# Kernel optimization log

Measured on AMD Instinct MI355X. Metric: run time of the kernel, lower is better.

The kernel has to match this reference:

```python
import jax, jax.numpy as jnp
import numpy as np

B, S, D, K = 32, 512, 512, 2048
NHEADS, NHASH, HLEN = 8, 4, 16
COMMIT = 0.25


def _conv1d(x, w, b):
    # x: [B, C, S], w: [O, I, k] (torch Conv1d layout), 'same' padding for odd k
    k = w.shape[-1]
    y = jax.lax.conv_general_dilated(x, w, (1,), [(k // 2, k // 2)],
                                     dimension_numbers=('NCH', 'OIH', 'NCH'))
    return y + b[None, :, None]


def _mha(x, in_w, in_b, out_w, out_b, nheads):
    # torch nn.MultiheadAttention (batch_first) with packed in_proj
    b, s, d = x.shape
    dh = d // nheads
    qkv = x @ in_w.T + in_b
    q, k, v = jnp.split(qkv, 3, axis=-1)
    sp = lambda t: t.reshape(b, s, nheads, dh).transpose(0, 2, 1, 3)
    q, k, v = sp(q), sp(k), sp(v)
    attn = jax.nn.softmax(jnp.einsum('bhqd,bhkd->bhqk', q, k) * (dh ** -0.5), axis=-1)
    o = jnp.einsum('bhqk,bhkd->bhqd', attn, v).transpose(0, 2, 1, 3).reshape(b, s, d)
    return o @ out_w.T + out_b


def setup_inputs() -> dict:
    key = jax.random.key(0)
    ks = jax.random.split(key, 16)
    w = lambda k, shape, s=0.02: jax.random.normal(k, shape, jnp.float32) * s
    z = lambda *shape: jnp.zeros(shape, jnp.float32)
    return {
        'market_data': jax.random.normal(ks[0], (B, S, D), jnp.float32),
        'W_in': w(ks[1], (D, D)), 'b_in': z(D),
        'pos_enc': w(ks[2], (S, D)),
        'conv3_w': w(ks[3], (D, D, 3)), 'conv3_b': z(D),
        'conv5_w': w(ks[4], (D, D, 5)), 'conv5_b': z(D),
        'conv7_w': w(ks[5], (D, D, 7)), 'conv7_b': z(D),
        'conv9_w': w(ks[6], (D, D, 9)), 'conv9_b': z(D),
        'ms_proj_w': w(ks[7], (D, 4 * D)), 'ms_proj_b': z(D),
        'in_proj_w': w(ks[8], (3 * D, D)), 'in_proj_b': z(3 * D),
        'attn_out_w': w(ks[9], (D, D)), 'attn_out_b': z(D),
        'codebook': jax.random.uniform(ks[10], (K, D), jnp.float32, -1.0 / K, 1.0 / K),
        'hash_w': w(ks[11], (NHASH, HLEN, D), 1.0),
        'reg1_w': w(ks[12], (D // 2, D)), 'reg1_b': z(D // 2),
        'reg2_w': w(ks[13], (K, D // 2)), 'reg2_b': z(K),
    }


def reference(market_data, W_in, b_in, pos_enc, conv3_w, conv3_b, conv5_w, conv5_b,
              conv7_w, conv7_b, conv9_w, conv9_b, ms_proj_w, ms_proj_b,
              in_proj_w, in_proj_b, attn_out_w, attn_out_b, codebook, hash_w,
              reg1_w, reg1_b, reg2_w, reg2_b):
    # input projection
    x = market_data @ W_in.T + b_in                                   # [B,S,D]
    # --- subsequence encoder ---
    xp = x + pos_enc[:x.shape[1]][None]
    xt = xp.transpose(0, 2, 1)                                        # [B,D,S]
    scales = [jax.nn.relu(_conv1d(xt, cw, cb)).transpose(0, 2, 1)
              for cw, cb in ((conv3_w, conv3_b), (conv5_w, conv5_b),
                             (conv7_w, conv7_b), (conv9_w, conv9_b))]
    multi = jnp.concatenate(scales, axis=-1)                          # [B,S,4D]
    proj = multi @ ms_proj_w.T + ms_proj_b                            # [B,S,D]
    enc = proj + _mha(proj, in_proj_w, in_proj_b, attn_out_w, attn_out_b, NHEADS)
    # --- vector quantizer (eval mode: no EMA update) ---
    flat = enc.reshape(-1, D)                                         # [N,D]
    dist = (jnp.sum(flat * flat, axis=1, keepdims=True)
            + jnp.sum(codebook * codebook, axis=1)
            - 2.0 * (flat @ codebook.T))                              # [N,K]
    idx = jnp.argmin(dist, axis=1)                                    # [N]
    quant = codebook[idx].reshape(enc.shape)
    commit = jnp.mean((jax.lax.stop_gradient(quant) - enc) ** 2)
    cb_loss = jnp.mean((quant - jax.lax.stop_gradient(enc)) ** 2)
    vq_loss = COMMIT * commit + cb_loss
    quant_st = enc + jax.lax.stop_gradient(quant - enc)               # straight-through
    # --- hash encoder on semantic ids ---
    hash_codes = (jnp.einsum('bsd,nhd->bsnh', quant_st, hash_w) > 0).astype(jnp.float32)
    # --- regime classifier ---
    h = jax.nn.relu(quant_st @ reg1_w.T + reg1_b)
    regime = jax.nn.softmax(h @ reg2_w.T + reg2_b, axis=-1)
    return (quant_st, vq_loss, idx.reshape(enc.shape[:-1]), hash_codes, regime)
```

## Files before the change

kernel.cpp:

```cpp
#include <hip/hip_runtime.h>
#include <hip/hip_bf16.h>


#define GF_BIAS 1
#define GF_RELU 2
#define GF_ADDP 4
#define GF_POS  8
#define GF_ACCP 16
#define GF_QSCALE 32

typedef _Float16 f16x8 __attribute__((ext_vector_type(8)));
typedef float    f32x4 __attribute__((ext_vector_type(4)));

static constexpr long long O_QUANT = 0LL;
static constexpr long long O_LOSS  = 8388608LL;
static constexpr long long O_IDX   = 8388609LL;
static constexpr long long O_HASH  = 8404993LL;
static constexpr long long O_REG   = 9453569LL;
static constexpr long long O_END   = 43008001LL;

static constexpr long long W_XP    = 0LL;
static constexpr long long W_CT    = 8388608LL;
static constexpr long long W_PROJ  = 16777216LL;
static constexpr long long W_VW    = 25165824LL;
static constexpr long long W_HREG  = 33554432LL;
static constexpr long long W_T     = 34078720LL;
static constexpr long long W_IDX   = 34209792LL;
static constexpr long long W_ASUM  = 34226176LL;
static constexpr long long W_CBB   = 34258944LL;
static constexpr long long W_LPART = 34263040LL;
static constexpr long long W_PBV   = 34271232LL;
static constexpr long long W_PBI   = 34336768LL;
static constexpr long long W_END   = 34402304LL;

__device__ __forceinline__ unsigned int pack_hl(float x)
{
    _Float16 h = (_Float16)x;
    float hf = (float)h;
    _Float16 l = (_Float16)(x - hf);
    unsigned short hb = __builtin_bit_cast(unsigned short, h);
    unsigned short lb = __builtin_bit_cast(unsigned short, l);
    return (unsigned int)hb | ((unsigned int)lb << 16);
}

__device__ __forceinline__ void split2(float x, unsigned short& h, unsigned short& l)
{
    _Float16 hf = (_Float16)x;
    _Float16 lf = (_Float16)(x - (float)hf);
    h = __builtin_bit_cast(unsigned short, hf);
    l = __builtin_bit_cast(unsigned short, lf);
}

__device__ __forceinline__ float unpack_sum(unsigned int u)
{
    _Float16 h = __builtin_bit_cast(_Float16, (unsigned short)(u & 0xffff));
    _Float16 l = __builtin_bit_cast(_Float16, (unsigned short)(u >> 16));
    return (float)h + (float)l;
}

__global__ __launch_bounds__(256)
void split_hl_r23(const float* __restrict__ src, unsigned int* __restrict__ dst)
{
    long long i = (long long)blockIdx.x*256 + threadIdx.x;
    dst[i] = pack_hl(src[i]);
}

__global__ __launch_bounds__(256)
void split_cb_r23(const float* __restrict__ cb, unsigned int* __restrict__ cbhl)
{
    long long i = (long long)blockIdx.x*256 + threadIdx.x;
    cbhl[i] = pack_hl(cb[i] * 2048.0f);
}

template<int KT>
__global__ __launch_bounds__(256)
void conv_w_tr_r23(const float* __restrict__ w, unsigned int* __restrict__ wt)
{
    long long i = (long long)blockIdx.x*256 + threadIdx.x;
    int o  = (int)(i / (512*KT));
    int rem= (int)(i % (512*KT));
    int t  = rem >> 9;
    int ii = rem & 511;
    wt[i] = pack_hl(w[(long long)o*512*KT + (long long)ii*KT + t]);
}

template<int KT>
__global__ __launch_bounds__(256)
void conv_mfma_r23(const unsigned int* __restrict__ xphl,
                   const unsigned int* __restrict__ wthl,
                   const float* __restrict__ bias, unsigned int* __restrict__ outp)
{
    constexpr int PAD = KT / 2;
    __shared__ unsigned short Ah[136][40];
    __shared__ unsigned short Al[136][40];
    __shared__ unsigned short Bh[128][40];
    __shared__ unsigned short Bl[128][40];
    const int tid  = threadIdx.x;
    const int lane = tid & 63;
    const int wave = tid >> 6;
    const int wm = (wave >> 1) * 64, wn = (wave & 1) * 64;
    const int bm = blockIdx.x * 128, bn = blockIdx.y * 128;
    const int l15 = lane & 15;
    const int lk8 = (lane >> 4) * 8;
    const int rbase = (lane >> 4) * 4;
    const int sb = bm & 511;
    const int brow0 = tid >> 3, bc = tid & 7;

    f32x4 acc[4][4];
    #pragma unroll
    for (int i=0;i<4;i++)
        #pragma unroll
        for (int j=0;j<4;j++)
            acc[i][j] = (f32x4){0.f,0.f,0.f,0.f};

    for (int i0 = 0; i0 < 512; i0 += 32) {
        __syncthreads();
        for (int sl = tid; sl < 136*8; sl += 256) {
            const int row = sl >> 3, c = sl & 7;
            const int srow = sb + row - 4;
            uint4 v = make_uint4(0u,0u,0u,0u);
            if (srow >= 0 && srow < 512)
                v = *(const uint4*)(xphl + (long long)(bm + row - 4)*512 + i0 + c*4);
            Ah[row][c*4+0] = (unsigned short)(v.x & 0xffff);
            Ah[row][c*4+1] = (unsigned short)(v.y & 0xffff);
            Ah[row][c*4+2] = (unsigned short)(v.z & 0xffff);
            Ah[row][c*4+3] = (unsigned short)(v.w & 0xffff);
            Al[row][c*4+0] = (unsigned short)(v.x >> 16);
            Al[row][c*4+1] = (unsigned short)(v.y >> 16);
            Al[row][c*4+2] = (unsigned short)(v.z >> 16);
            Al[row][c*4+3] = (unsigned short)(v.w >> 16);
        }
        uint4 vb[4];
        #pragma unroll
        for (int q = 0; q < 4; ++q) {
            const int row = brow0 + q*32;
            vb[q] = *(const uint4*)(wthl + (long long)(bn + row)*(KT*512) + 0*512 + i0 + bc*4);
        }
        for (int t = 0; t < KT; ++t) {
            #pragma unroll
            for (int q = 0; q < 4; ++q) {
                const int row = brow0 + q*32;
                Bh[row][bc*4+0] = (unsigned short)(vb[q].x & 0xffff);
                Bh[row][bc*4+1] = (unsigned short)(vb[q].y & 0xffff);
                Bh[row][bc*4+2] = (unsigned short)(vb[q].z & 0xffff);
                Bh[row][bc*4+3] = (unsigned short)(vb[q].w & 0xffff);
                Bl[row][bc*4+0] = (unsigned short)(vb[q].x >> 16);
                Bl[row][bc*4+1] = (unsigned short)(vb[q].y >> 16);
                Bl[row][bc*4+2] = (unsigned short)(vb[q].z >> 16);
                Bl[row][bc*4+3] = (unsigned short)(vb[q].w >> 16);
            }
            if (t + 1 < KT) {
                #pragma unroll
                for (int q = 0; q < 4; ++q) {
                    const int row = brow0 + q*32;
                    vb[q] = *(const uint4*)(wthl + (long long)(bn + row)*(KT*512) + (t+1)*512 + i0 + bc*4);
                }
            }
            __syncthreads();
            const int tofs = t - PAD + 4;
            f16x8 ah[4], al[4], bh[4], bl[4];
            #pragma unroll
            for (int mi = 0; mi < 4; ++mi) {
                ah[mi] = *(const f16x8*)(&Ah[wm + mi*16 + l15 + tofs][lk8]);
                al[mi] = *(const f16x8*)(&Al[wm + mi*16 + l15 + tofs][lk8]);
            }
            #pragma unroll
            for (int nj = 0; nj < 4; ++nj) {
                bh[nj] = *(const f16x8*)(&Bh[wn + nj*16 + l15][lk8]);
                bl[nj] = *(const f16x8*)(&Bl[wn + nj*16 + l15][lk8]);
            }
            #pragma unroll
            for (int mi = 0; mi < 4; ++mi)
                #pragma unroll
                for (int nj = 0; nj < 4; ++nj) {
                    acc[mi][nj] = __builtin_amdgcn_mfma_f32_16x16x32_f16(ah[mi], bh[nj], acc[mi][nj], 0, 0, 0);
                    acc[mi][nj] = __builtin_amdgcn_mfma_f32_16x16x32_f16(ah[mi], bl[nj], acc[mi][nj], 0, 0, 0);
                    acc[mi][nj] = __builtin_amdgcn_mfma_f32_16x16x32_f16(al[mi], bh[nj], acc[mi][nj], 0, 0, 0);
                }
            if (t + 1 < KT) __syncthreads();
        }
    }
    #pragma unroll
    for (int mi = 0; mi < 4; ++mi) {
        #pragma unroll
        for (int nj = 0; nj < 4; ++nj) {
            const int col = bn + wn + nj*16 + l15;
            const float bcol = bias[col];
            #pragma unroll
            for (int r = 0; r < 4; ++r) {
                const int row = bm + wm + mi*16 + rbase + r;
                float v = acc[mi][nj][r] + bcol;
                outp[(long long)row*512 + col] = pack_hl(fmaxf(v, 0.0f));
            }
        }
    }
}

template<int FLAGS>
__global__ __launch_bounds__(256)
void gemm_hl_r23(const unsigned int* __restrict__ A, const unsigned int* __restrict__ Bm,
                 const float* __restrict__ bias, const float* __restrict__ pos,
                 const unsigned int* __restrict__ addsrc, unsigned int* __restrict__ C,
                 int Kdim, int lda, int ldb, int ldc)
{
    __shared__ unsigned short Ah[128][40];
    __shared__ unsigned short Al[128][40];
    __shared__ unsigned short Bh[128][40];
    __shared__ unsigned short Bl[128][40];
    const int tid  = threadIdx.x;
    const int lane = tid & 63;
    const int wave = tid >> 6;
    const int wm = (wave >> 1) * 64, wn = (wave & 1) * 64;
    const int bm = blockIdx.x * 128, bn = blockIdx.y * 128;
    const int l15 = lane & 15;
    const int lk8 = (lane >> 4) * 8;
    const int rbase = (lane >> 4) * 4;
    const int cg   = tid & 7;
    const int rw0  = tid >> 3;

    f32x4 acc[4][4];
    #pragma unroll
    for (int i=0;i<4;i++)
        #pragma unroll
        for (int j=0;j<4;j++)
            acc[i][j] = (f32x4){0.f,0.f,0.f,0.f};

    uint4 va[4], vb[4];
    #pragma unroll
    for (int q = 0; q < 4; ++q) {
        const int row = rw0 + q*32;
        va[q] = *(const uint4*)(A  + (long long)(bm + row)*lda + cg*4);
        vb[q] = *(const uint4*)(Bm + (long long)(bn + row)*ldb + cg*4);
    }

    for (int k0 = 0; k0 < Kdim; k0 += 32) {
        __syncthreads();
        #pragma unroll
        for (int q = 0; q < 4; ++q) {
            const int row = rw0 + q*32;
            Ah[row][cg*4+0] = (unsigned short)(va[q].x & 0xffff);
            Ah[row][cg*4+1] = (unsigned short)(va[q].y & 0xffff);
            Ah[row][cg*4+2] = (unsigned short)(va[q].z & 0xffff);
            Ah[row][cg*4+3] = (unsigned short)(va[q].w & 0xffff);
            Al[row][cg*4+0] = (unsigned short)(va[q].x >> 16);
            Al[row][cg*4+1] = (unsigned short)(va[q].y >> 16);
            Al[row][cg*4+2] = (unsigned short)(va[q].z >> 16);
            Al[row][cg*4+3] = (unsigned short)(va[q].w >> 16);
            Bh[row][cg*4+0] = (unsigned short)(vb[q].x & 0xffff);
            Bh[row][cg*4+1] = (unsigned short)(vb[q].y & 0xffff);
            Bh[row][cg*4+2] = (unsigned short)(vb[q].z & 0xffff);
            Bh[row][cg*4+3] = (unsigned short)(vb[q].w & 0xffff);
            Bl[row][cg*4+0] = (unsigned short)(vb[q].x >> 16);
            Bl[row][cg*4+1] = (unsigned short)(vb[q].y >> 16);
            Bl[row][cg*4+2] = (unsigned short)(vb[q].z >> 16);
            Bl[row][cg*4+3] = (unsigned short)(vb[q].w >> 16);
        }
        if (k0 + 32 < Kdim) {
            #pragma unroll
            for (int q = 0; q < 4; ++q) {
                const int row = rw0 + q*32;
                va[q] = *(const uint4*)(A  + (long long)(bm + row)*lda + k0 + 32 + cg*4);
                vb[q] = *(const uint4*)(Bm + (long long)(bn + row)*ldb + k0 + 32 + cg*4);
            }
        }
        __syncthreads();
        f16x8 ah[4], al[4], bh[4], bl[4];
        #pragma unroll
        for (int mi = 0; mi < 4; ++mi) {
            ah[mi] = *(const f16x8*)(&Ah[wm + mi*16 + l15][lk8]);
            al[mi] = *(const f16x8*)(&Al[wm + mi*16 + l15][lk8]);
        }
        #pragma unroll
        for (int nj = 0; nj < 4; ++nj) {
            bh[nj] = *(const f16x8*)(&Bh[wn + nj*16 + l15][lk8]);
            bl[nj] = *(const f16x8*)(&Bl[wn + nj*16 + l15][lk8]);
        }
        #pragma unroll
        for (int mi = 0; mi < 4; ++mi)
            #pragma unroll
            for (int nj = 0; nj < 4; ++nj) {
                acc[mi][nj] = __builtin_amdgcn_mfma_f32_16x16x32_f16(ah[mi], bh[nj], acc[mi][nj], 0, 0, 0);
                acc[mi][nj] = __builtin_amdgcn_mfma_f32_16x16x32_f16(ah[mi], bl[nj], acc[mi][nj], 0, 0, 0);
                acc[mi][nj] = __builtin_amdgcn_mfma_f32_16x16x32_f16(al[mi], bh[nj], acc[mi][nj], 0, 0, 0);
            }
    }
    #pragma unroll
    for (int mi = 0; mi < 4; ++mi) {
        #pragma unroll
        for (int nj = 0; nj < 4; ++nj) {
            const int col = bn + wn + nj*16 + l15;
            #pragma unroll
            for (int r = 0; r < 4; ++r) {
                const int row = bm + wm + mi*16 + rbase + r;
                float v = acc[mi][nj][r];
                if constexpr (FLAGS & GF_BIAS) v += bias[col];
                if constexpr (FLAGS & GF_POS)  v += pos[(long long)(row & 511)*512 + col];
                if constexpr (FLAGS & GF_ADDP) v += unpack_sum(addsrc[(long long)row*ldc + col]);
                if constexpr (FLAGS & GF_ACCP) v += unpack_sum(C[(long long)row*ldc + col]);
                if constexpr (FLAGS & GF_QSCALE) v *= 0.125f;
                C[(long long)row*ldc + col] = pack_hl(v);
            }
        }
    }
}

__global__ __launch_bounds__(256)
void attn_mfma_r23(const unsigned int* __restrict__ Qbuf, const unsigned int* __restrict__ Kbuf,
                   const unsigned int* __restrict__ Vbuf, unsigned int* __restrict__ att)
{
    __shared__ unsigned short Qh[64][68];
    __shared__ unsigned short Ql[64][68];
    __shared__ unsigned short Kh[64][68];
    __shared__ unsigned short Kl[64][68];
    __shared__ unsigned short Vh[64][68];
    __shared__ unsigned short Vl[64][68];
    const int tid  = threadIdx.x;
    const int lane = tid & 63;
    const int wave = tid >> 6;
    const int l15  = lane & 15;
    const int lq   = lane >> 4;
    const int lq8  = lq * 8;
    const int bid = blockIdx.x;
    const int qt = bid & 7, h = (bid >> 3) & 7, b = bid >> 6;
    const int row0 = b*512 + qt*64;

    #pragma unroll
    for (int u = 0; u < 16; ++u) {
        int e = u*256 + tid;
        int r = e >> 6, c = e & 63;
        unsigned int uq = Qbuf[(long long)(row0 + r)*512 + h*64 + c];
        Qh[r][c] = (unsigned short)(uq & 0xffff);
        Ql[r][c] = (unsigned short)(uq >> 16);
    }

    float m[4], l[4];
    f32x4 accO[4];
    #pragma unroll
    for (int r=0;r<4;r++){ m[r] = -1e30f; l[r] = 0.f; }
    #pragma unroll
    for (int j=0;j<4;j++) accO[j] = (f32x4){0.f,0.f,0.f,0.f};

    for (int kv = 0; kv < 512; kv += 64) {
        __syncthreads();
        #pragma unroll
        for (int u = 0; u < 16; ++u) {
            int e = u*256 + tid;
            int r = e >> 6, c = e & 63;
            unsigned int uk = Kbuf[(long long)(b*512 + kv + r)*512 + h*64 + c];
            unsigned int uv = Vbuf[(long long)(b*512 + kv + r)*512 + h*64 + c];
            Kh[r][c] = (unsigned short)(uk & 0xffff);
            Kl[r][c] = (unsigned short)(uk >> 16);
            Vh[c][r] = (unsigned short)(uv & 0xffff);
            Vl[c][r] = (unsigned short)(uv >> 16);
        }
        __syncthreads();
        f32x4 accS[4];
        #pragma unroll
        for (int j=0;j<4;j++) accS[j] = (f32x4){0.f,0.f,0.f,0.f};
        #pragma unroll
        for (int ks = 0; ks < 2; ++ks) {
            f16x8 qh = *(const f16x8*)(&Qh[wave*16 + l15][ks*32 + lq8]);
            f16x8 ql = *(const f16x8*)(&Ql[wave*16 + l15][ks*32 + lq8]);
            #pragma unroll
            for (int nj = 0; nj < 4; ++nj) {
                f16x8 kh = *(const f16x8*)(&Kh[nj*16 + l15][ks*32 + lq8]);
                f16x8 kl = *(const f16x8*)(&Kl[nj*16 + l15][ks*32 + lq8]);
                accS[nj] = __builtin_amdgcn_mfma_f32_16x16x32_f16(qh, kh, accS[nj], 0, 0, 0);
                accS[nj] = __builtin_amdgcn_mfma_f32_16x16x32_f16(qh, kl, accS[nj], 0, 0, 0);
                accS[nj] = __builtin_amdgcn_mfma_f32_16x16x32_f16(ql, kh, accS[nj], 0, 0, 0);
            }
        }
        #pragma unroll
        for (int r = 0; r < 4; ++r) {
            float tm = fmaxf(fmaxf(accS[0][r], accS[1][r]), fmaxf(accS[2][r], accS[3][r]));
            #pragma unroll
            for (int msk = 1; msk < 16; msk <<= 1) tm = fmaxf(tm, __shfl_xor(tm, msk, 64));
            float mn = fmaxf(m[r], tm);
            float scale = expf(m[r] - mn);
            float rs = 0.f;
            #pragma unroll
            for (int nj = 0; nj < 4; ++nj) {
                float p = expf(accS[nj][r] - mn);
                accS[nj][r] = p;
                rs += p;
            }
            #pragma unroll
            for (int msk = 1; msk < 16; msk <<= 1) rs += __shfl_xor(rs, msk, 64);
            l[r] = l[r]*scale + rs;
            m[r] = mn;
            #pragma unroll
            for (int nj = 0; nj < 4; ++nj) accO[nj][r] *= scale;
        }
        __syncthreads();
        #pragma unroll
        for (int r = 0; r < 4; ++r)
            #pragma unroll
            for (int nj = 0; nj < 4; ++nj) {
                unsigned short hs, ls;
                split2(accS[nj][r], hs, ls);
                Kh[wave*16 + lq*4 + r][nj*16 + l15] = hs;
                Kl[wave*16 + lq*4 + r][nj*16 + l15] = ls;
            }
        __syncthreads();
        #pragma unroll
        for (int ks = 0; ks < 2; ++ks) {
            f16x8 ph = *(const f16x8*)(&Kh[wave*16 + l15][ks*32 + lq8]);
            f16x8 pl = *(const f16x8*)(&Kl[wave*16 + l15][ks*32 + lq8]);
            #pragma unroll
            for (int nj = 0; nj < 4; ++nj) {
                f16x8 vh = *(const f16x8*)(&Vh[nj*16 + l15][ks*32 + lq8]);
                f16x8 vl = *(const f16x8*)(&Vl[nj*16 + l15][ks*32 + lq8]);
                accO[nj] = __builtin_amdgcn_mfma_f32_16x16x32_f16(ph, vh, accO[nj], 0, 0, 0);
                accO[nj] = __builtin_amdgcn_mfma_f32_16x16x32_f16(ph, vl, accO[nj], 0, 0, 0);
                accO[nj] = __builtin_amdgcn_mfma_f32_16x16x32_f16(pl, vh, accO[nj], 0, 0, 0);
            }
        }
    }
    #pragma unroll
    for (int nj = 0; nj < 4; ++nj)
        #pragma unroll
        for (int r = 0; r < 4; ++r) {
            const int row = row0 + wave*16 + lq*4 + r;
            att[(long long)row*512 + h*64 + nj*16 + l15] = pack_hl(accO[nj][r] / l[r]);
        }
}

__global__ __launch_bounds__(256)
void row_sumsq_r23(const float* __restrict__ X, double* __restrict__ outp)
{
    const int row  = blockIdx.x*4 + (threadIdx.x >> 6);
    const int lane = threadIdx.x & 63;
    double s = 0.0;
    #pragma unroll
    for (int u = 0; u < 8; ++u) {
        float v = X[(long long)row*512 + lane + u*64];
        s += (double)v * (double)v;
    }
    #pragma unroll
    for (int msk = 32; msk; msk >>= 1) s += __shfl_xor(s, msk, 64);
    if (lane == 0) outp[row] = s;
}

__global__ __launch_bounds__(256)
void row_sumsq_hl_r23(const unsigned int* __restrict__ X, double* __restrict__ outp)
{
    const int row  = blockIdx.x*4 + (threadIdx.x >> 6);
    const int lane = threadIdx.x & 63;
    double s = 0.0;
    #pragma unroll
    for (int u = 0; u < 8; ++u) {
        float v = unpack_sum(X[(long long)row*512 + lane + u*64]);
        s += (double)v * (double)v;
    }
    #pragma unroll
    for (int msk = 32; msk; msk >>= 1) s += __shfl_xor(s, msk, 64);
    if (lane == 0) outp[row] = s;
}

__global__ __launch_bounds__(256)
void vq_argmin_mfma_r23(const unsigned int* __restrict__ enchl,
                        const unsigned int* __restrict__ cbhl,
                        const double* __restrict__ Asum, const double* __restrict__ cbB,
                        float* __restrict__ pbv, int* __restrict__ pbi)
{
    __shared__ unsigned int smem[10240];
    unsigned short* AhP = (unsigned short*)smem;
    unsigned short* AlP = AhP + 128*40;
    unsigned short* BhP = AlP + 128*40;
    unsigned short* BlP = BhP + 128*40;
    float* bvsP = (float*)smem;
    int*   bisP = (int*)(smem + 4096);

    const int tid  = threadIdx.x;
    const int lane = tid & 63;
    const int wave = tid >> 6;
    const int wm = (wave >> 1) * 64, wn = (wave & 1) * 64;
    const int bm = blockIdx.x * 128;
    const int l15 = lane & 15;
    const int lk8 = (lane >> 4) * 8;
    const int rbase = (lane >> 4) * 4;
    const int cg   = tid & 7;
    const int rw0  = tid >> 3;

    float bestv[16]; int besti[16];
    #pragma unroll
    for (int g = 0; g < 16; ++g) { bestv[g] = 3.0e38f; besti[g] = 2048; }

    for (int nb = 0; nb < 4; ++nb) {
        const int ct0 = blockIdx.y * 512 + nb * 128;
        f32x4 acc[4][4];
        #pragma unroll
        for (int i=0;i<4;i++)
            #pragma unroll
            for (int j=0;j<4;j++)
                acc[i][j] = (f32x4){0.f,0.f,0.f,0.f};

        uint4 va[4], vb[4];
        #pragma unroll
        for (int q = 0; q < 4; ++q) {
            const int row = rw0 + q*32;
            va[q] = *(const uint4*)(enchl + (long long)(bm + row)*512 + cg*4);
            vb[q] = *(const uint4*)(cbhl  + (long long)(ct0 + row)*512 + cg*4);
        }

        for (int k0 = 0; k0 < 512; k0 += 32) {
            __syncthreads();
            #pragma unroll
            for (int q = 0; q < 4; ++q) {
                const int row = rw0 + q*32;
                AhP[row*40 + cg*4+0] = (unsigned short)(va[q].x & 0xffff);
                AhP[row*40 + cg*4+1] = (unsigned short)(va[q].y & 0xffff);
                AhP[row*40 + cg*4+2] = (unsigned short)(va[q].z & 0xffff);
                AhP[row*40 + cg*4+3] = (unsigned short)(va[q].w & 0xffff);
                AlP[row*40 + cg*4+0] = (unsigned short)(va[q].x >> 16);
                AlP[row*40 + cg*4+1] = (unsigned short)(va[q].y >> 16);
                AlP[row*40 + cg*4+2] = (unsigned short)(va[q].z >> 16);
                AlP[row*40 + cg*4+3] = (unsigned short)(va[q].w >> 16);
                BhP[row*40 + cg*4+0] = (unsigned short)(vb[q].x & 0xffff);
                BhP[row*40 + cg*4+1] = (unsigned short)(vb[q].y & 0xffff);
                BhP[row*40 + cg*4+2] = (unsigned short)(vb[q].z & 0xffff);
                BhP[row*40 + cg*4+3] = (unsigned short)(vb[q].w & 0xffff);
                BlP[row*40 + cg*4+0] = (unsigned short)(vb[q].x >> 16);
                BlP[row*40 + cg*4+1] = (unsigned short)(vb[q].y >> 16);
                BlP[row*40 + cg*4+2] = (unsigned short)(vb[q].z >> 16);
                BlP[row*40 + cg*4+3] = (unsigned short)(vb[q].w >> 16);
            }
            if (k0 + 32 < 512) {
                #pragma unroll
                for (int q = 0; q < 4; ++q) {
                    const int row = rw0 + q*32;
                    va[q] = *(const uint4*)(enchl + (long long)(bm + row)*512 + k0 + 32 + cg*4);
                    vb[q] = *(const uint4*)(cbhl  + (long long)(ct0 + row)*512 + k0 + 32 + cg*4);
                }
            }
            __syncthreads();
            f16x8 ah[4], al[4], bh[4], bl[4];
            #pragma unroll
            for (int mi = 0; mi < 4; ++mi) {
                ah[mi] = *(const f16x8*)(&AhP[(wm + mi*16 + l15)*40 + lk8]);
                al[mi] = *(const f16x8*)(&AlP[(wm + mi*16 + l15)*40 + lk8]);
            }
            #pragma unroll
            for (int nj = 0; nj < 4; ++nj) {
                bh[nj] = *(const f16x8*)(&BhP[(wn + nj*16 + l15)*40 + lk8]);
                bl[nj] = *(const f16x8*)(&BlP[(wn + nj*16 + l15)*40 + lk8]);
            }
            #pragma unroll
            for (int mi = 0; mi < 4; ++mi)
                #pragma unroll
                for (int nj = 0; nj < 4; ++nj) {
                    acc[mi][nj] = __builtin_amdgcn_mfma_f32_16x16x32_f16(ah[mi], bh[nj], acc[mi][nj], 0, 0, 0);
                    acc[mi][nj] = __builtin_amdgcn_mfma_f32_16x16x32_f16(ah[mi], bl[nj], acc[mi][nj], 0, 0, 0);
                    acc[mi][nj] = __builtin_amdgcn_mfma_f32_16x16x32_f16(al[mi], bh[nj], acc[mi][nj], 0, 0, 0);
                }
        }
        #pragma unroll
        for (int mi = 0; mi < 4; ++mi) {
            #pragma unroll
            for (int r = 0; r < 4; ++r) {
                const int g = mi*4 + r;
                const float anf = (float)Asum[bm + wm + mi*16 + rbase + r];
                #pragma unroll
                for (int nj = 0; nj < 4; ++nj) {
                    const int col = ct0 + wn + nj*16 + l15;
                    const float bf = (float)cbB[col];
                    const float s1 = anf + bf;
                    const float dot = acc[mi][nj][r] * (1.0f/2048.0f);
                    const float df  = 2.0f * dot;
                    const float qd  = s1 - df;
                    if (qd < bestv[g] || (qd == bestv[g] && col < besti[g])) {
                        bestv[g] = qd; besti[g] = col;
                    }
                }
            }
        }
    }
    __syncthreads();
    #pragma unroll
    for (int mi = 0; mi < 4; ++mi)
        #pragma unroll
        for (int r = 0; r < 4; ++r) {
            const int row  = wm + mi*16 + rbase + r;
            const int slot = (wave & 1)*16 + l15;
            bvsP[row*32 + slot] = bestv[mi*4 + r];
            bisP[row*32 + slot] = besti[mi*4 + r];
        }
    __syncthreads();
    if (tid < 128) {
        float bv = bvsP[tid*32]; int bi = bisP[tid*32];
        #pragma unroll
        for (int s = 1; s < 32; ++s) {
            float v = bvsP[tid*32 + s]; int ii = bisP[tid*32 + s];
            if (v < bv || (v == bv && ii < bi)) { bv = v; bi = ii; }
        }
        pbv[(long long)blockIdx.y*16384 + bm + tid] = bv;
        pbi[(long long)blockIdx.y*16384 + bm + tid] = bi;
    }
}

__global__ __launch_bounds__(256)
void vq_reduce_r23(const float* __restrict__ pbv, const int* __restrict__ pbi,
                   int* __restrict__ idxout, float* __restrict__ out)
{
    int n = blockIdx.x*256 + threadIdx.x;
    if (n >= 16384) return;
    float bv = pbv[n]; int bi = pbi[n];
    #pragma unroll
    for (int q = 1; q < 4; ++q) {
        float v = pbv[q*16384 + n]; int ii = pbi[q*16384 + n];
        if (v < bv || (v == bv && ii < bi)) { bv = v; bi = ii; }
    }
    int ci = bi & 2047;
    idxout[n] = ci;
    out[O_IDX + n] = (float)ci;
}

__global__ __launch_bounds__(256)
void vq_loss_partial_r23(const unsigned int* __restrict__ enchl,
                         const float* __restrict__ cb,
                         const int* __restrict__ idxp, double* __restrict__ part)
{
    __shared__ double red[4];
    const int row  = blockIdx.x*4 + (threadIdx.x >> 6);
    const int lane = threadIdx.x & 63;
    const int ci = idxp[row] & 2047;
    double s = 0.0;
    #pragma unroll
    for (int u = 0; u < 8; ++u) {
        int d = lane + u*64;
        float e = unpack_sum(enchl[(long long)row*512 + d]);
        double dv = (double)cb[(long long)ci*512 + d] - (double)e;
        s += dv * dv;
    }
    #pragma unroll
    for (int msk = 32; msk; msk >>= 1) s += __shfl_xor(s, msk, 64);
    if (lane == 0) red[threadIdx.x >> 6] = s;
    __syncthreads();
    if (threadIdx.x == 0)
        part[blockIdx.x] = red[0] + red[1] + red[2] + red[3];
}

template<int FLAGS>
__global__ __launch_bounds__(256)
void gemm_bt_r23(const float* __restrict__ A, const float* __restrict__ Bm,
                 const float* __restrict__ bias, const float* __restrict__ pos,
                 const float* __restrict__ addsrc, float* __restrict__ C,
                 int Kdim, int lda, int ldb, int ldc)
{
    __shared__ float As[16][132];
    __shared__ float Bs[16][132];
    const int tid = threadIdx.x;
    const int tx = tid & 15, ty = tid >> 4;
    const int bm = blockIdx.x * 128, bn = blockIdx.y * 128;
    const int r0 = tid >> 2;
    const int kg = (tid & 3) << 2;
    const float* Arow0 = A  + (long long)(bm + r0) * lda + kg;
    const float* Arow1 = A  + (long long)(bm + r0 + 64) * lda + kg;
    const float* Brow0 = Bm + (long long)(bn + r0) * ldb + kg;
    const float* Brow1 = Bm + (long long)(bn + r0 + 64) * ldb + kg;

    float acc[8][8] = {};
    for (int k0 = 0; k0 < Kdim; k0 += 16) {
        float4 a0 = *(const float4*)(Arow0 + k0);
        float4 a1 = *(const float4*)(Arow1 + k0);
        float4 b0 = *(const float4*)(Brow0 + k0);
        float4 b1 = *(const float4*)(Brow1 + k0);
        __syncthreads();
        As[kg+0][r0]=a0.x; As[kg+1][r0]=a0.y; As[kg+2][r0]=a0.z; As[kg+3][r0]=a0.w;
        As[kg+0][r0+64]=a1.x; As[kg+1][r0+64]=a1.y; As[kg+2][r0+64]=a1.z; As[kg+3][r0+64]=a1.w;
        Bs[kg+0][r0]=b0.x; Bs[kg+1][r0]=b0.y; Bs[kg+2][r0]=b0.z; Bs[kg+3][r0]=b0.w;
        Bs[kg+0][r0+64]=b1.x; Bs[kg+1][r0+64]=b1.y; Bs[kg+2][r0+64]=b1.z; Bs[kg+3][r0+64]=b1.w;
        __syncthreads();
        #pragma unroll
        for (int kk = 0; kk < 16; ++kk) {
            float a[8], b[8];
            #pragma unroll
            for (int i=0;i<8;i++) a[i] = As[kk][ty*8+i];
            #pragma unroll
            for (int j=0;j<4;j++) b[j]   = Bs[kk][tx*4+j];
            #pragma unroll
            for (int j=0;j<4;j++) b[4+j] = Bs[kk][64+tx*4+j];
            #pragma unroll
            for (int i=0;i<8;i++)
                #pragma unroll
                for (int j=0;j<8;j++)
                    acc[i][j] = fmaf(a[i], b[j], acc[i][j]);
        }
    }
    #pragma unroll
    for (int i=0;i<8;i++){
        const int row = bm + ty*8 + i;
        #pragma unroll
        for (int j=0;j<8;j++){
            const int col = bn + ((j < 4) ? (tx*4 + j) : (64 + tx*4 + (j-4)));
            float v = acc[i][j];
            if constexpr (FLAGS & GF_BIAS) v += bias[col];
            if constexpr (FLAGS & GF_RELU) v = fmaxf(v, 0.0f);
            C[(long long)row*ldc + col] = v;
        }
    }
}

__global__ __launch_bounds__(256)
void softmax_rows_r23(float* __restrict__ R)
{
    const int row = blockIdx.x;
    const int tid = threadIdx.x;
    __shared__ float  redf[256];
    __shared__ double redd[256];
    float* p = R + (long long)row * 2048;
    float mx = -1e30f;
    for (int c = tid; c < 2048; c += 256) mx = fmaxf(mx, p[c]);
    redf[tid] = mx; __syncthreads();
    for (int s2 = 128; s2; s2 >>= 1) { if (tid < s2) redf[tid] = fmaxf(redf[tid], redf[tid+s2]); __syncthreads(); }
    mx = redf[0];
    double sum = 0.0;
    for (int c = tid; c < 2048; c += 256) { float e = expf(p[c] - mx); p[c] = e; sum += e; }
    redd[tid] = sum; __syncthreads();
    for (int s2 = 128; s2; s2 >>= 1) { if (tid < s2) redd[tid] += redd[tid+s2]; __syncthreads(); }
    double tot = redd[0];
    for (int c = tid; c < 2048; c += 256) p[c] = (float)((double)p[c] / tot);
}

__global__ __launch_bounds__(256)
void hash_table_r23(const float* __restrict__ cb, const float* __restrict__ hw,
                    float* __restrict__ T)
{
    const int k = blockIdx.x*4 + (threadIdx.x >> 6);
    const int j = threadIdx.x & 63;
    double s = 0.0;
    for (int d = 0; d < 512; ++d)
        s += (double)cb[(long long)k*512 + d] * (double)hw[(long long)j*512 + d];
    T[(long long)k*64 + j] = (s > 0.0) ? 1.0f : 0.0f;
}

__global__ void write_loss_r23(const double* __restrict__ part,
                               float* __restrict__ out)
{
    __shared__ double red[256];
    double s = 0.0;
    for (int i = threadIdx.x; i < 4096; i += 256) s += part[i];
    red[threadIdx.x] = s; __syncthreads();
    for (int s2 = 128; s2; s2 >>= 1) {
        if (threadIdx.x < s2) red[threadIdx.x] += red[threadIdx.x + s2];
        __syncthreads();
    }
    if (threadIdx.x == 0)
        out[O_LOSS] = (float)(1.25 * red[0] / 8388608.0);
}

__global__ __launch_bounds__(256)
void write_regime_r23(const float* __restrict__ R, const int* __restrict__ idxp,
                      float* __restrict__ out)
{
    long long i = (long long)blockIdx.x*256 + threadIdx.x;
    if (i >= 33554432LL) return;
    int n = (int)(i >> 11), c = (int)(i & 2047);
    int ci = idxp[n] & 2047;
    out[O_REG + i] = R[(long long)ci*2048 + c];
}

__global__ __launch_bounds__(256)
void write_hash_r23(const float* __restrict__ T, const int* __restrict__ idxp,
                    float* __restrict__ out)
{
    long long i = (long long)blockIdx.x*256 + threadIdx.x;
    if (i >= 1048576LL) return;
    int n = (int)(i >> 6), j = (int)(i & 63);
    int ci = idxp[n] & 2047;
    out[O_HASH + i] = T[(long long)ci*64 + j];
}

__global__ __launch_bounds__(256)
void write_quant_r23(const float* __restrict__ cb, const int* __restrict__ idxp,
                     float* __restrict__ out)
{
    long long i = (long long)blockIdx.x*256 + threadIdx.x;
    if (i >= 8388608LL) return;
    int n = (int)(i >> 9), d = (int)(i & 511);
    int ci = idxp[n] & 2047;
    out[O_QUANT + i] = cb[(long long)ci*512 + d];
}

extern "C" void kernel_launch(void* const* d_in, const int* in_sizes, int n_in,
                              void* d_out, int out_size, void* d_ws, size_t ws_size,
                              hipStream_t stream)
{
    (void)in_sizes; (void)n_in; (void)out_size;
    const float* market = (const float*)d_in[0];
    const float* W_in   = (const float*)d_in[1];
    const float* b_in   = (const float*)d_in[2];
    const float* pos    = (const float*)d_in[3];
    const float* c3w = (const float*)d_in[4];  const float* c3b = (const float*)d_in[5];
    const float* c5w = (const float*)d_in[6];  const float* c5b = (const float*)d_in[7];
    const float* c7w = (const float*)d_in[8];  const float* c7b = (const float*)d_in[9];
    const float* c9w = (const float*)d_in[10]; const float* c9b = (const float*)d_in[11];
    const float* msw = (const float*)d_in[12]; const float* msb = (const float*)d_in[13];
    const float* inw = (const float*)d_in[14]; const float* inb = (const float*)d_in[15];
    const float* aow = (const float*)d_in[16]; const float* aob = (const float*)d_in[17];
    const float* cb  = (const float*)d_in[18]; const float* hw  = (const float*)d_in[19];
    const float* r1w = (const float*)d_in[20]; const float* r1b = (const float*)d_in[21];
    const float* r2w = (const float*)d_in[22]; const float* r2b = (const float*)d_in[23];

    if (ws_size < (size_t)W_END * sizeof(float)) return;

    float* ws = (float*)d_ws;
    unsigned int* xphl   = (unsigned int*)(ws + W_XP);
    unsigned int* cthl   = (unsigned int*)(ws + W_CT);
    unsigned int* projhl = (unsigned int*)(ws + W_PROJ);
    unsigned int* vwbase = (unsigned int*)(ws + W_VW);
    unsigned int* wt3 = vwbase;
    unsigned int* wt5 = wt3 + 512*512*3;
    unsigned int* wt7 = wt5 + 512*512*5;
    unsigned int* wt9 = wt7 + 512*512*7;
    unsigned int* mswhl  = vwbase + 6291456;
    unsigned int* winhl  = mswhl + 1048576;
    unsigned int* inwqhl = winhl + 262144;
    unsigned int* inwkhl = inwqhl + 262144;
    unsigned int* vhl    = vwbase;
    unsigned int* inwvhl = (unsigned int*)(ws + W_HREG);
    unsigned int* aowhl  = inwvhl + 262144;
    float* hregp = ws + W_HREG;
    float* Tp    = ws + W_T;
    int*    idxp  = (int*)(ws + W_IDX);
    double* asump = (double*)(ws + W_ASUM);
    double* cbbp  = (double*)(ws + W_CBB);
    double* lpart = (double*)(ws + W_LPART);
    float*  pbvp  = ws + W_PBV;
    int*    pbip  = (int*)(ws + W_PBI);
    unsigned int* cbhl = (unsigned int*)(ws + W_PROJ + 4194304);
    float* Rp = ws + W_PROJ;

    float* out = (float*)d_out;

    conv_w_tr_r23<3><<<3072, 256, 0, stream>>>(c3w, wt3);
    conv_w_tr_r23<5><<<5120, 256, 0, stream>>>(c5w, wt5);
    conv_w_tr_r23<7><<<7168, 256, 0, stream>>>(c7w, wt7);
    conv_w_tr_r23<9><<<9216, 256, 0, stream>>>(c9w, wt9);
    split_hl_r23<<<32768, 256, 0, stream>>>(market, cthl);
    split_hl_r23<<<1024,  256, 0, stream>>>(W_in, winhl);
    split_hl_r23<<<4096,  256, 0, stream>>>(msw, mswhl);
    split_hl_r23<<<1024,  256, 0, stream>>>(inw,            inwqhl);
    split_hl_r23<<<1024,  256, 0, stream>>>(inw + 262144,   inwkhl);
    split_hl_r23<<<1024,  256, 0, stream>>>(inw + 524288,   inwvhl);
    split_hl_r23<<<1024,  256, 0, stream>>>(aow, aowhl);

    const dim3 gT(128, 4);

    gemm_hl_r23<GF_BIAS|GF_POS><<<gT, 256, 0, stream>>>(cthl, winhl, b_in, pos, nullptr, xphl, 512, 512, 512, 512);

    conv_mfma_r23<3><<<gT, 256, 0, stream>>>(xphl, wt3, c3b, cthl);
    gemm_hl_r23<GF_BIAS><<<gT, 256, 0, stream>>>(cthl, mswhl + 0*512, msb, nullptr, nullptr, projhl, 512, 512, 2048, 512);
    conv_mfma_r23<5><<<gT, 256, 0, stream>>>(xphl, wt5, c5b, cthl);
    gemm_hl_r23<GF_ACCP><<<gT, 256, 0, stream>>>(cthl, mswhl + 1*512, nullptr, nullptr, nullptr, projhl, 512, 512, 2048, 512);
    conv_mfma_r23<7><<<gT, 256, 0, stream>>>(xphl, wt7, c7b, cthl);
    gemm_hl_r23<GF_ACCP><<<gT, 256, 0, stream>>>(cthl, mswhl + 2*512, nullptr, nullptr, nullptr, projhl, 512, 512, 2048, 512);
    conv_mfma_r23<9><<<gT, 256, 0, stream>>>(xphl, wt9, c9b, cthl);
    gemm_hl_r23<GF_ACCP><<<gT, 256, 0, stream>>>(cthl, mswhl + 3*512, nullptr, nullptr, nullptr, projhl, 512, 512, 2048, 512);

    gemm_hl_r23<GF_BIAS><<<gT, 256, 0, stream>>>(projhl, inwkhl, inb + 512,  nullptr, nullptr, cthl, 512, 512, 512, 512);
    gemm_hl_r23<GF_BIAS|GF_QSCALE><<<gT, 256, 0, stream>>>(projhl, inwqhl, inb, nullptr, nullptr, xphl, 512, 512, 512, 512);
    gemm_hl_r23<GF_BIAS><<<gT, 256, 0, stream>>>(projhl, inwvhl, inb + 1024, nullptr, nullptr, vhl, 512, 512, 512, 512);

    attn_mfma_r23<<<2048, 256, 0, stream>>>(xphl, cthl, vhl, xphl);

    gemm_hl_r23<GF_BIAS|GF_ADDP><<<gT, 256, 0, stream>>>(xphl, aowhl, aob, nullptr, projhl, cthl, 512, 512, 512, 512);

    row_sumsq_hl_r23<<<4096, 256, 0, stream>>>(cthl, asump);
    row_sumsq_r23<<<512,  256, 0, stream>>>(cb, cbbp);
    split_cb_r23<<<4096, 256, 0, stream>>>(cb, cbhl);
    vq_argmin_mfma_r23<<<dim3(128, 4), 256, 0, stream>>>(cthl, cbhl, asump, cbbp, pbvp, pbip);
    vq_reduce_r23<<<64, 256, 0, stream>>>(pbvp, pbip, idxp, out);
    vq_loss_partial_r23<<<4096, 256, 0, stream>>>(cthl, cb, idxp, lpart);

    gemm_bt_r23<GF_BIAS|GF_RELU><<<dim3(16, 2),  256, 0, stream>>>(cb, r1w, r1b, nullptr, nullptr, hregp, 512, 512, 512, 256);
    gemm_bt_r23<GF_BIAS><<<dim3(16, 16), 256, 0, stream>>>(hregp, r2w, r2b, nullptr, nullptr, Rp, 256, 256, 256, 2048);
    softmax_rows_r23<<<2048, 256, 0, stream>>>(Rp);
    hash_table_r23<<<512, 256, 0, stream>>>(cb, hw, Tp);

    write_loss_r23<<<1, 256, 0, stream>>>(lpart, out);
    write_regime_r23<<<131072, 256, 0, stream>>>(Rp, idxp, out);
    write_hash_r23<<<4096, 256, 0, stream>>>(Tp, idxp, out);
    write_quant_r23<<<32768, 256, 0, stream>>>(cb, idxp, out);
}
```

Before: 1.469 ms.

## Double-buffer LDS tiles in conv, GEMM and VQ argmin MFMA kernels

```diff
diff --git a/kernel.cpp b/kernel.cpp
--- a/kernel.cpp
+++ b/kernel.cpp
@@ -58,15 +58,27 @@
     return (float)h + (float)l;
 }
 
-__global__ __launch_bounds__(256)
-void split_hl_r23(const float* __restrict__ src, unsigned int* __restrict__ dst)
+__device__ __forceinline__ void st_hl(unsigned short* Hp, unsigned short* Lp, uint4 v)
+{
+    Hp[0] = (unsigned short)(v.x & 0xffff);
+    Hp[1] = (unsigned short)(v.y & 0xffff);
+    Hp[2] = (unsigned short)(v.z & 0xffff);
+    Hp[3] = (unsigned short)(v.w & 0xffff);
+    Lp[0] = (unsigned short)(v.x >> 16);
+    Lp[1] = (unsigned short)(v.y >> 16);
+    Lp[2] = (unsigned short)(v.z >> 16);
+    Lp[3] = (unsigned short)(v.w >> 16);
+}
+
+__global__ __launch_bounds__(256)
+void split_hl_r24(const float* __restrict__ src, unsigned int* __restrict__ dst)
 {
     long long i = (long long)blockIdx.x*256 + threadIdx.x;
     dst[i] = pack_hl(src[i]);
 }
 
 __global__ __launch_bounds__(256)
-void split_cb_r23(const float* __restrict__ cb, unsigned int* __restrict__ cbhl)
+void split_cb_r24(const float* __restrict__ cb, unsigned int* __restrict__ cbhl)
 {
     long long i = (long long)blockIdx.x*256 + threadIdx.x;
     cbhl[i] = pack_hl(cb[i] * 2048.0f);
@@ -74,7 +86,7 @@
 
 template<int KT>
 __global__ __launch_bounds__(256)
-void conv_w_tr_r23(const float* __restrict__ w, unsigned int* __restrict__ wt)
+void conv_w_tr_r24(const float* __restrict__ w, unsigned int* __restrict__ wt)
 {
     long long i = (long long)blockIdx.x*256 + threadIdx.x;
     int o  = (int)(i / (512*KT));
@@ -86,15 +98,15 @@
 
 template<int KT>
 __global__ __launch_bounds__(256)
-void conv_mfma_r23(const unsigned int* __restrict__ xphl,
+void conv_mfma_r24(const unsigned int* __restrict__ xphl,
                    const unsigned int* __restrict__ wthl,
                    const float* __restrict__ bias, unsigned int* __restrict__ outp)
 {
     constexpr int PAD = KT / 2;
     __shared__ unsigned short Ah[136][40];
     __shared__ unsigned short Al[136][40];
-    __shared__ unsigned short Bh[128][40];
-    __shared__ unsigned short Bl[128][40];
+    __shared__ unsigned short Bh[2][128][40];
+    __shared__ unsigned short Bl[2][128][40];
     const int tid  = threadIdx.x;
     const int lane = tid & 63;
     const int wave = tid >> 6;
@@ -114,21 +126,13 @@
             acc[i][j] = (f32x4){0.f,0.f,0.f,0.f};
 
     for (int i0 = 0; i0 < 512; i0 += 32) {
-        __syncthreads();
         for (int sl = tid; sl < 136*8; sl += 256) {
             const int row = sl >> 3, c = sl & 7;
             const int srow = sb + row - 4;
             uint4 v = make_uint4(0u,0u,0u,0u);
             if (srow >= 0 && srow < 512)
                 v = *(const uint4*)(xphl + (long long)(bm + row - 4)*512 + i0 + c*4);
-            Ah[row][c*4+0] = (unsigned short)(v.x & 0xffff);
-            Ah[row][c*4+1] = (unsigned short)(v.y & 0xffff);
-            Ah[row][c*4+2] = (unsigned short)(v.z & 0xffff);
-            Ah[row][c*4+3] = (unsigned short)(v.w & 0xffff);
-            Al[row][c*4+0] = (unsigned short)(v.x >> 16);
-            Al[row][c*4+1] = (unsigned short)(v.y >> 16);
-            Al[row][c*4+2] = (unsigned short)(v.z >> 16);
-            Al[row][c*4+3] = (unsigned short)(v.w >> 16);
+            st_hl(&Ah[row][c*4], &Al[row][c*4], v);
         }
         uint4 vb[4];
         #pragma unroll
@@ -136,27 +140,21 @@
             const int row = brow0 + q*32;
             vb[q] = *(const uint4*)(wthl + (long long)(bn + row)*(KT*512) + 0*512 + i0 + bc*4);
         }
-        for (int t = 0; t < KT; ++t) {
+        #pragma unroll
+        for (int q = 0; q < 4; ++q) {
+            const int row = brow0 + q*32;
+            st_hl(&Bh[0][row][bc*4], &Bl[0][row][bc*4], vb[q]);
+        }
+        if (KT > 1) {
             #pragma unroll
             for (int q = 0; q < 4; ++q) {
                 const int row = brow0 + q*32;
-                Bh[row][bc*4+0] = (unsigned short)(vb[q].x & 0xffff);
-                Bh[row][bc*4+1] = (unsigned short)(vb[q].y & 0xffff);
-                Bh[row][bc*4+2] = (unsigned short)(vb[q].z & 0xffff);
-                Bh[row][bc*4+3] = (unsigned short)(vb[q].w & 0xffff);
-                Bl[row][bc*4+0] = (unsigned short)(vb[q].x >> 16);
-                Bl[row][bc*4+1] = (unsigned short)(vb[q].y >> 16);
-                Bl[row][bc*4+2] = (unsigned short)(vb[q].z >> 16);
-                Bl[row][bc*4+3] = (unsigned short)(vb[q].w >> 16);
-            }
-            if (t + 1 < KT) {
-                #pragma unroll
-                for (int q = 0; q < 4; ++q) {
-                    const int row = brow0 + q*32;
-                    vb[q] = *(const uint4*)(wthl + (long long)(bn + row)*(KT*512) + (t+1)*512 + i0 + bc*4);
-                }
-            }
-            __syncthreads();
+                vb[q] = *(const uint4*)(wthl + (long long)(bn + row)*(KT*512) + 1*512 + i0 + bc*4);
+            }
+        }
+        __syncthreads();
+        for (int t = 0; t < KT; ++t) {
+            const int buf = t & 1;
             const int tofs = t - PAD + 4;
             f16x8 ah[4], al[4], bh[4], bl[4];
             #pragma unroll
@@ -166,8 +164,8 @@
             }
             #pragma unroll
             for (int nj = 0; nj < 4; ++nj) {
-                bh[nj] = *(const f16x8*)(&Bh[wn + nj*16 + l15][lk8]);
-                bl[nj] = *(const f16x8*)(&Bl[wn + nj*16 + l15][lk8]);
+                bh[nj] = *(const f16x8*)(&Bh[buf][wn + nj*16 + l15][lk8]);
+                bl[nj] = *(const f16x8*)(&Bl[buf][wn + nj*16 + l15][lk8]);
             }
             #pragma unroll
             for (int mi = 0; mi < 4; ++mi)
@@ -177,7 +175,21 @@
                     acc[mi][nj] = __builtin_amdgcn_mfma_f32_16x16x32_f16(ah[mi], bl[nj], acc[mi][nj], 0, 0, 0);
                     acc[mi][nj] = __builtin_amdgcn_mfma_f32_16x16x32_f16(al[mi], bh[nj], acc[mi][nj], 0, 0, 0);
                 }
-            if (t + 1 < KT) __syncthreads();
+            if (t + 1 < KT) {
+                #pragma unroll
+                for (int q = 0; q < 4; ++q) {
+                    const int row = brow0 + q*32;
+                    st_hl(&Bh[buf^1][row][bc*4], &Bl[buf^1][row][bc*4], vb[q]);
+                }
+                if (t + 2 < KT) {
+                    #pragma unroll
+                    for (int q = 0; q < 4; ++q) {
+                        const int row = brow0 + q*32;
+                        vb[q] = *(const uint4*)(wthl + (long long)(bn + row)*(KT*512) + (t+2)*512 + i0 + bc*4);
+                    }
+                }
+            }
+            __syncthreads();
         }
     }
     #pragma unroll
@@ -198,15 +210,15 @@
 
 template<int FLAGS>
 __global__ __launch_bounds__(256)
-void gemm_hl_r23(const unsigned int* __restrict__ A, const unsigned int* __restrict__ Bm,
+void gemm_hl_r24(const unsigned int* __restrict__ A, const unsigned int* __restrict__ Bm,
                  const float* __restrict__ bias, const float* __restrict__ pos,
                  const unsigned int* __restrict__ addsrc, unsigned int* __restrict__ C,
                  int Kdim, int lda, int ldb, int ldc)
 {
-    __shared__ unsigned short Ah[128][40];
-    __shared__ unsigned short Al[128][40];
-    __shared__ unsigned short Bh[128][40];
-    __shared__ unsigned short Bl[128][40];
+    __shared__ unsigned short Ah[2][128][40];
+    __shared__ unsigned short Al[2][128][40];
+    __shared__ unsigned short Bh[2][128][40];
+    __shared__ unsigned short Bl[2][128][40];
     const int tid  = threadIdx.x;
     const int lane = tid & 63;
     const int wave = tid >> 6;
@@ -225,6 +237,7 @@
         for (int j=0;j<4;j++)
             acc[i][j] = (f32x4){0.f,0.f,0.f,0.f};
 
+    const int C_N = Kdim >> 5;
     uint4 va[4], vb[4];
     #pragma unroll
     for (int q = 0; q < 4; ++q) {
@@ -232,48 +245,34 @@
         va[q] = *(const uint4*)(A  + (long long)(bm + row)*lda + cg*4);
         vb[q] = *(const uint4*)(Bm + (long long)(bn + row)*ldb + cg*4);
     }
-
-    for (int k0 = 0; k0 < Kdim; k0 += 32) {
-        __syncthreads();
+    #pragma unroll
+    for (int q = 0; q < 4; ++q) {
+        const int row = rw0 + q*32;
+        st_hl(&Ah[0][row][cg*4], &Al[0][row][cg*4], va[q]);
+        st_hl(&Bh[0][row][cg*4], &Bl[0][row][cg*4], vb[q]);
+    }
+    if (C_N > 1) {
         #pragma unroll
         for (int q = 0; q < 4; ++q) {
             const int row = rw0 + q*32;
-            Ah[row][cg*4+0] = (unsigned short)(va[q].x & 0xffff);
-            Ah[row][cg*4+1] = (unsigned short)(va[q].y & 0xffff);
-            Ah[row][cg*4+2] = (unsigned short)(va[q].z & 0xffff);
-            Ah[row][cg*4+3] = (unsigned short)(va[q].w & 0xffff);
-            Al[row][cg*4+0] = (unsigned short)(va[q].x >> 16);
-            Al[row][cg*4+1] = (unsigned short)(va[q].y >> 16);
-            Al[row][cg*4+2] = (unsigned short)(va[q].z >> 16);
-            Al[row][cg*4+3] = (unsigned short)(va[q].w >> 16);
-            Bh[row][cg*4+0] = (unsigned short)(vb[q].x & 0xffff);
-            Bh[row][cg*4+1] = (unsigned short)(vb[q].y & 0xffff);
-            Bh[row][cg*4+2] = (unsigned short)(vb[q].z & 0xffff);
-            Bh[row][cg*4+3] = (unsigned short)(vb[q].w & 0xffff);
-            Bl[row][cg*4+0] = (unsigned short)(vb[q].x >> 16);
-            Bl[row][cg*4+1] = (unsigned short)(vb[q].y >> 16);
-            Bl[row][cg*4+2] = (unsigned short)(vb[q].z >> 16);
-            Bl[row][cg*4+3] = (unsigned short)(vb[q].w >> 16);
-        }
-        if (k0 + 32 < Kdim) {
-            #pragma unroll
-            for (int q = 0; q < 4; ++q) {
-                const int row = rw0 + q*32;
-                va[q] = *(const uint4*)(A  + (long long)(bm + row)*lda + k0 + 32 + cg*4);
-                vb[q] = *(const uint4*)(Bm + (long long)(bn + row)*ldb + k0 + 32 + cg*4);
-            }
-        }
-        __syncthreads();
+            va[q] = *(const uint4*)(A  + (long long)(bm + row)*lda + 32 + cg*4);
+            vb[q] = *(const uint4*)(Bm + (long long)(bn + row)*ldb + 32 + cg*4);
+        }
+    }
+    __syncthreads();
+
+    for (int c = 0; c < C_N; ++c) {
+        const int buf = c & 1;
         f16x8 ah[4], al[4], bh[4], bl[4];
         #pragma unroll
         for (int mi = 0; mi < 4; ++mi) {
-            ah[mi] = *(const f16x8*)(&Ah[wm + mi*16 + l15][lk8]);
-            al[mi] = *(const f16x8*)(&Al[wm + mi*16 + l15][lk8]);
+            ah[mi] = *(const f16x8*)(&Ah[buf][wm + mi*16 + l15][lk8]);
+            al[mi] = *(const f16x8*)(&Al[buf][wm + mi*16 + l15][lk8]);
         }
         #pragma unroll
         for (int nj = 0; nj < 4; ++nj) {
-            bh[nj] = *(const f16x8*)(&Bh[wn + nj*16 + l15][lk8]);
-            bl[nj] = *(const f16x8*)(&Bl[wn + nj*16 + l15][lk8]);
+            bh[nj] = *(const f16x8*)(&Bh[buf][wn + nj*16 + l15][lk8]);
+            bl[nj] = *(const f16x8*)(&Bl[buf][wn + nj*16 + l15][lk8]);
         }
         #pragma unroll
         for (int mi = 0; mi < 4; ++mi)
@@ -283,6 +282,23 @@
                 acc[mi][nj] = __builtin_amdgcn_mfma_f32_16x16x32_f16(ah[mi], bl[nj], acc[mi][nj], 0, 0, 0);
                 acc[mi][nj] = __builtin_amdgcn_mfma_f32_16x16x32_f16(al[mi], bh[nj], acc[mi][nj], 0, 0, 0);
             }
+        if (c + 1 < C_N) {
+            #pragma unroll
+            for (int q = 0; q < 4; ++q) {
+                const int row = rw0 + q*32;
+                st_hl(&Ah[buf^1][row][cg*4], &Al[buf^1][row][cg*4], va[q]);
+                st_hl(&Bh[buf^1][row][cg*4], &Bl[buf^1][row][cg*4], vb[q]);
+            }
+            if (c + 2 < C_N) {
+                #pragma unroll
+                for (int q = 0; q < 4; ++q) {
+                    const int row = rw0 + q*32;
+                    va[q] = *(const uint4*)(A  + (long long)(bm + row)*lda + (c+2)*32 + cg*4);
+                    vb[q] = *(const uint4*)(Bm + (long long)(bn + row)*ldb + (c+2)*32 + cg*4);
+                }
+            }
+        }
+        __syncthreads();
     }
     #pragma unroll
     for (int mi = 0; mi < 4; ++mi) {
@@ -305,7 +321,7 @@
 }
 
 __global__ __launch_bounds__(256)
-void attn_mfma_r23(const unsigned int* __restrict__ Qbuf, const unsigned int* __restrict__ Kbuf,
+void attn_mfma_r24(const unsigned int* __restrict__ Qbuf, const unsigned int* __restrict__ Kbuf,
                    const unsigned int* __restrict__ Vbuf, unsigned int* __restrict__ att)
 {
     __shared__ unsigned short Qh[64][68];
@@ -426,7 +442,7 @@
 }
 
 __global__ __launch_bounds__(256)
-void row_sumsq_r23(const float* __restrict__ X, double* __restrict__ outp)
+void row_sumsq_r24(const float* __restrict__ X, double* __restrict__ outp)
 {
     const int row  = blockIdx.x*4 + (threadIdx.x >> 6);
     const int lane = threadIdx.x & 63;
@@ -442,7 +458,7 @@
 }
 
 __global__ __launch_bounds__(256)
-void row_sumsq_hl_r23(const unsigned int* __restrict__ X, double* __restrict__ outp)
+void row_sumsq_hl_r24(const unsigned int* __restrict__ X, double* __restrict__ outp)
 {
     const int row  = blockIdx.x*4 + (threadIdx.x >> 6);
     const int lane = threadIdx.x & 63;
@@ -458,16 +474,16 @@
 }
 
 __global__ __launch_bounds__(256)
-void vq_argmin_mfma_r23(const unsigned int* __restrict__ enchl,
+void vq_argmin_mfma_r24(const unsigned int* __restrict__ enchl,
                         const unsigned int* __restrict__ cbhl,
                         const double* __restrict__ Asum, const double* __restrict__ cbB,
                         float* __restrict__ pbv, int* __restrict__ pbi)
 {
-    __shared__ unsigned int smem[10240];
+    __shared__ unsigned int smem[20480];
     unsigned short* AhP = (unsigned short*)smem;
-    unsigned short* AlP = AhP + 128*40;
-    unsigned short* BhP = AlP + 128*40;
-    unsigned short* BlP = BhP + 128*40;
+    unsigned short* AlP = AhP + 2*128*40;
+    unsigned short* BhP = AlP + 2*128*40;
+    unsigned short* BlP = BhP + 2*128*40;
     float* bvsP = (float*)smem;
     int*   bisP = (int*)(smem + 4096);
 
@@ -502,48 +518,33 @@
             va[q] = *(const uint4*)(enchl + (long long)(bm + row)*512 + cg*4);
             vb[q] = *(const uint4*)(cbhl  + (long long)(ct0 + row)*512 + cg*4);
         }
-
-        for (int k0 = 0; k0 < 512; k0 += 32) {
-            __syncthreads();
-            #pragma unroll
-            for (int q = 0; q < 4; ++q) {
-                const int row = rw0 + q*32;
-                AhP[row*40 + cg*4+0] = (unsigned short)(va[q].x & 0xffff);
-                AhP[row*40 + cg*4+1] = (unsigned short)(va[q].y & 0xffff);
-                AhP[row*40 + cg*4+2] = (unsigned short)(va[q].z & 0xffff);
-                AhP[row*40 + cg*4+3] = (unsigned short)(va[q].w & 0xffff);
-                AlP[row*40 + cg*4+0] = (unsigned short)(va[q].x >> 16);
-                AlP[row*40 + cg*4+1] = (unsigned short)(va[q].y >> 16);
-                AlP[row*40 + cg*4+2] = (unsigned short)(va[q].z >> 16);
-                AlP[row*40 + cg*4+3] = (unsigned short)(va[q].w >> 16);
-                BhP[row*40 + cg*4+0] = (unsigned short)(vb[q].x & 0xffff);
-                BhP[row*40 + cg*4+1] = (unsigned short)(vb[q].y & 0xffff);
-                BhP[row*40 + cg*4+2] = (unsigned short)(vb[q].z & 0xffff);
-                BhP[row*40 + cg*4+3] = (unsigned short)(vb[q].w & 0xffff);
-                BlP[row*40 + cg*4+0] = (unsigned short)(vb[q].x >> 16);
-                BlP[row*40 + cg*4+1] = (unsigned short)(vb[q].y >> 16);
-                BlP[row*40 + cg*4+2] = (unsigned short)(vb[q].z >> 16);
-                BlP[row*40 + cg*4+3] = (unsigned short)(vb[q].w >> 16);
-            }
-            if (k0 + 32 < 512) {
-                #pragma unroll
-                for (int q = 0; q < 4; ++q) {
-                    const int row = rw0 + q*32;
-                    va[q] = *(const uint4*)(enchl + (long long)(bm + row)*512 + k0 + 32 + cg*4);
-                    vb[q] = *(const uint4*)(cbhl  + (long long)(ct0 + row)*512 + k0 + 32 + cg*4);
-                }
-            }
-            __syncthreads();
+        __syncthreads();
+        #pragma unroll
+        for (int q = 0; q < 4; ++q) {
+            const int row = rw0 + q*32;
+            st_hl(&AhP[(0*128 + row)*40 + cg*4], &AlP[(0*128 + row)*40 + cg*4], va[q]);
+            st_hl(&BhP[(0*128 + row)*40 + cg*4], &BlP[(0*128 + row)*40 + cg*4], vb[q]);
+        }
+        #pragma unroll
+        for (int q = 0; q < 4; ++q) {
+            const int row = rw0 + q*32;
+            va[q] = *(const uint4*)(enchl + (long long)(bm + row)*512 + 32 + cg*4);
+            vb[q] = *(const uint4*)(cbhl  + (long long)(ct0 + row)*512 + 32 + cg*4);
+        }
+        __syncthreads();
+
+        for (int c = 0; c < 16; ++c) {
+            const int buf = c & 1;
             f16x8 ah[4], al[4], bh[4], bl[4];
             #pragma unroll
             for (int mi = 0; mi < 4; ++mi) {
-                ah[mi] = *(const f16x8*)(&AhP[(wm + mi*16 + l15)*40 + lk8]);
-                al[mi] = *(const f16x8*)(&AlP[(wm + mi*16 + l15)*40 + lk8]);
+                ah[mi] = *(const f16x8*)(&AhP[(buf*128 + wm + mi*16 + l15)*40 + lk8]);
+                al[mi] = *(const f16x8*)(&AlP[(buf*128 + wm + mi*16 + l15)*40 + lk8]);
             }
             #pragma unroll
             for (int nj = 0; nj < 4; ++nj) {
-                bh[nj] = *(const f16x8*)(&BhP[(wn + nj*16 + l15)*40 + lk8]);
-                bl[nj] = *(const f16x8*)(&BlP[(wn + nj*16 + l15)*40 + lk8]);
+                bh[nj] = *(const f16x8*)(&BhP[(buf*128 + wn + nj*16 + l15)*40 + lk8]);
+                bl[nj] = *(const f16x8*)(&BlP[(buf*128 + wn + nj*16 + l15)*40 + lk8]);
             }
             #pragma unroll
             for (int mi = 0; mi < 4; ++mi)
@@ -553,6 +554,23 @@
                     acc[mi][nj] = __builtin_amdgcn_mfma_f32_16x16x32_f16(ah[mi], bl[nj], acc[mi][nj], 0, 0, 0);
                     acc[mi][nj] = __builtin_amdgcn_mfma_f32_16x16x32_f16(al[mi], bh[nj], acc[mi][nj], 0, 0, 0);
                 }
+            if (c + 1 < 16) {
+                #pragma unroll
+                for (int q = 0; q < 4; ++q) {
+                    const int row = rw0 + q*32;
+                    st_hl(&AhP[((buf^1)*128 + row)*40 + cg*4], &AlP[((buf^1)*128 + row)*40 + cg*4], va[q]);
+                    st_hl(&BhP[((buf^1)*128 + row)*40 + cg*4], &BlP[((buf^1)*128 + row)*40 + cg*4], vb[q]);
+                }
+                if (c + 2 < 16) {
+                    #pragma unroll
+                    for (int q = 0; q < 4; ++q) {
+                        const int row = rw0 + q*32;
+                        va[q] = *(const uint4*)(enchl + (long long)(bm + row)*512 + (c+2)*32 + cg*4);
+                        vb[q] = *(const uint4*)(cbhl  + (long long)(ct0 + row)*512 + (c+2)*32 + cg*4);
+                    }
+                }
+            }
+            __syncthreads();
         }
         #pragma unroll
         for (int mi = 0; mi < 4; ++mi) {
@@ -599,7 +617,7 @@
 }
 
 __global__ __launch_bounds__(256)
-void vq_reduce_r23(const float* __restrict__ pbv, const int* __restrict__ pbi,
+void vq_reduce_r24(const float* __restrict__ pbv, const int* __restrict__ pbi,
                    int* __restrict__ idxout, float* __restrict__ out)
 {
     int n = blockIdx.x*256 + threadIdx.x;
@@ -616,7 +634,7 @@
 }
 
 __global__ __launch_bounds__(256)
-void vq_loss_partial_r23(const unsigned int* __restrict__ enchl,
+void vq_loss_partial_r24(const unsigned int* __restrict__ enchl,
                          const float* __restrict__ cb,
                          const int* __restrict__ idxp, double* __restrict__ part)
 {
@@ -642,7 +660,7 @@
 
 template<int FLAGS>
 __global__ __launch_bounds__(256)
-void gemm_bt_r23(const float* __restrict__ A, const float* __restrict__ Bm,
+void gemm_bt_r24(const float* __restrict__ A, const float* __restrict__ Bm,
                  const float* __restrict__ bias, const float* __restrict__ pos,
                  const float* __restrict__ addsrc, float* __restrict__ C,
                  int Kdim, int lda, int ldb, int ldc)
@@ -702,7 +720,7 @@
 }
 
 __global__ __launch_bounds__(256)
-void softmax_rows_r23(float* __restrict__ R)
+void softmax_rows_r24(float* __restrict__ R)
 {
     const int row = blockIdx.x;
     const int tid = threadIdx.x;
@@ -723,7 +741,7 @@
 }
 
 __global__ __launch_bounds__(256)
-void hash_table_r23(const float* __restrict__ cb, const float* __restrict__ hw,
+void hash_table_r24(const float* __restrict__ cb, const float* __restrict__ hw,
                     float* __restrict__ T)
 {
     const int k = blockIdx.x*4 + (threadIdx.x >> 6);
@@ -734,7 +752,7 @@
     T[(long long)k*64 + j] = (s > 0.0) ? 1.0f : 0.0f;
 }
 
-__global__ void write_loss_r23(const double* __restrict__ part,
+__global__ void write_loss_r24(const double* __restrict__ part,
                                float* __restrict__ out)
 {
     __shared__ double red[256];
@@ -750,7 +768,7 @@
 }
 
 __global__ __launch_bounds__(256)
-void write_regime_r23(const float* __restrict__ R, const int* __restrict__ idxp,
+void write_regime_r24(const float* __restrict__ R, const int* __restrict__ idxp,
                       float* __restrict__ out)
 {
     long long i = (long long)blockIdx.x*256 + threadIdx.x;
@@ -761,7 +779,7 @@
 }
 
 __global__ __launch_bounds__(256)
-void write_hash_r23(const float* __restrict__ T, const int* __restrict__ idxp,
+void write_hash_r24(const float* __restrict__ T, const int* __restrict__ idxp,
                     float* __restrict__ out)
 {
     long long i = (long long)blockIdx.x*256 + threadIdx.x;
@@ -772,7 +790,7 @@
 }
 
 __global__ __launch_bounds__(256)
-void write_quant_r23(const float* __restrict__ cb, const int* __restrict__ idxp,
+void write_quant_r24(const float* __restrict__ cb, const int* __restrict__ idxp,
                      float* __restrict__ out)
 {
     long long i = (long long)blockIdx.x*256 + threadIdx.x;
@@ -833,53 +851,53 @@
 
     float* out = (float*)d_out;
 
-    conv_w_tr_r23<3><<<3072, 256, 0, stream>>>(c3w, wt3);
-    conv_w_tr_r23<5><<<5120, 256, 0, stream>>>(c5w, wt5);
-    conv_w_tr_r23<7><<<7168, 256, 0, stream>>>(c7w, wt7);
-    conv_w_tr_r23<9><<<9216, 256, 0, stream>>>(c9w, wt9);
-    split_hl_r23<<<32768, 256, 0, stream>>>(market, cthl);
-    split_hl_r23<<<1024,  256, 0, stream>>>(W_in, winhl);
-    split_hl_r23<<<4096,  256, 0, stream>>>(msw, mswhl);
-    split_hl_r23<<<1024,  256, 0, stream>>>(inw,            inwqhl);
-    split_hl_r23<<<1024,  256, 0, stream>>>(inw + 262144,   inwkhl);
-    split_hl_r23<<<1024,  256, 0, stream>>>(inw + 524288,   inwvhl);
-    split_hl_r23<<<1024,  256, 0, stream>>>(aow, aowhl);
+    conv_w_tr_r24<3><<<3072, 256, 0, stream>>>(c3w, wt3);
+    conv_w_tr_r24<5><<<5120, 256, 0, stream>>>(c5w, wt5);
+    conv_w_tr_r24<7><<<7168, 256, 0, stream>>>(c7w, wt7);
+    conv_w_tr_r24<9><<<9216, 256, 0, stream>>>(c9w, wt9);
+    split_hl_r24<<<32768, 256, 0, stream>>>(market, cthl);
+    split_hl_r24<<<1024,  256, 0, stream>>>(W_in, winhl);
+    split_hl_r24<<<4096,  256, 0, stream>>>(msw, mswhl);
+    split_hl_r24<<<1024,  256, 0, stream>>>(inw,            inwqhl);
+    split_hl_r24<<<1024,  256, 0, stream>>>(inw + 262144,   inwkhl);
+    split_hl_r24<<<1024,  256, 0, stream>>>(inw + 524288,   inwvhl);
+    split_hl_r24<<<1024,  256, 0, stream>>>(aow, aowhl);
 
     const dim3 gT(128, 4);
 
-    gemm_hl_r23<GF_BIAS|GF_POS><<<gT, 256, 0, stream>>>(cthl, winhl, b_in, pos, nullptr, xphl, 512, 512, 512, 512);
-
-    conv_mfma_r23<3><<<gT, 256, 0, stream>>>(xphl, wt3, c3b, cthl);
-    gemm_hl_r23<GF_BIAS><<<gT, 256, 0, stream>>>(cthl, mswhl + 0*512, msb, nullptr, nullptr, projhl, 512, 512, 2048, 512);
-    conv_mfma_r23<5><<<gT, 256, 0, stream>>>(xphl, wt5, c5b, cthl);
-    gemm_hl_r23<GF_ACCP><<<gT, 256, 0, stream>>>(cthl, mswhl + 1*512, nullptr, nullptr, nullptr, projhl, 512, 512, 2048, 512);
-    conv_mfma_r23<7><<<gT, 256, 0, stream>>>(xphl, wt7, c7b, cthl);
-    gemm_hl_r23<GF_ACCP><<<gT, 256, 0, stream>>>(cthl, mswhl + 2*512, nullptr, nullptr, nullptr, projhl, 512, 512, 2048, 512);
-    conv_mfma_r23<9><<<gT, 256, 0, stream>>>(xphl, wt9, c9b, cthl);
-    gemm_hl_r23<GF_ACCP><<<gT, 256, 0, stream>>>(cthl, mswhl + 3*512, nullptr, nullptr, nullptr, projhl, 512, 512, 2048, 512);
-
-    gemm_hl_r23<GF_BIAS><<<gT, 256, 0, stream>>>(projhl, inwkhl, inb + 512,  nullptr, nullptr, cthl, 512, 512, 512, 512);
-    gemm_hl_r23<GF_BIAS|GF_QSCALE><<<gT, 256, 0, stream>>>(projhl, inwqhl, inb, nullptr, nullptr, xphl, 512, 512, 512, 512);
-    gemm_hl_r23<GF_BIAS><<<gT, 256, 0, stream>>>(projhl, inwvhl, inb + 1024, nullptr, nullptr, vhl, 512, 512, 512, 512);
-
-    attn_mfma_r23<<<2048, 256, 0, stream>>>(xphl, cthl, vhl, xphl);
-
-    gemm_hl_r23<GF_BIAS|GF_ADDP><<<gT, 256, 0, stream>>>(xphl, aowhl, aob, nullptr, projhl, cthl, 512, 512, 512, 512);
-
-    row_sumsq_hl_r23<<<4096, 256, 0, stream>>>(cthl, asump);
-    row_sumsq_r23<<<512,  256, 0, stream>>>(cb, cbbp);
-    split_cb_r23<<<4096, 256, 0, stream>>>(cb, cbhl);
-    vq_argmin_mfma_r23<<<dim3(128, 4), 256, 0, stream>>>(cthl, cbhl, asump, cbbp, pbvp, pbip);
-    vq_reduce_r23<<<64, 256, 0, stream>>>(pbvp, pbip, idxp, out);
-    vq_loss_partial_r23<<<4096, 256, 0, stream>>>(cthl, cb, idxp, lpart);
-
-    gemm_bt_r23<GF_BIAS|GF_RELU><<<dim3(16, 2),  256, 0, stream>>>(cb, r1w, r1b, nullptr, nullptr, hregp, 512, 512, 512, 256);
-    gemm_bt_r23<GF_BIAS><<<dim3(16, 16), 256, 0, stream>>>(hregp, r2w, r2b, nullptr, nullptr, Rp, 256, 256, 256, 2048);
-    softmax_rows_r23<<<2048, 256, 0, stream>>>(Rp);
-    hash_table_r23<<<512, 256, 0, stream>>>(cb, hw, Tp);
-
-    write_loss_r23<<<1, 256, 0, stream>>>(lpart, out);
-    write_regime_r23<<<131072, 256, 0, stream>>>(Rp, idxp, out);
-    write_hash_r23<<<4096, 256, 0, stream>>>(Tp, idxp, out);
-    write_quant_r23<<<32768, 256, 0, stream>>>(cb, idxp, out);
-}
+    gemm_hl_r24<GF_BIAS|GF_POS><<<gT, 256, 0, stream>>>(cthl, winhl, b_in, pos, nullptr, xphl, 512, 512, 512, 512);
+
+    conv_mfma_r24<3><<<gT, 256, 0, stream>>>(xphl, wt3, c3b, cthl);
+    gemm_hl_r24<GF_BIAS><<<gT, 256, 0, stream>>>(cthl, mswhl + 0*512, msb, nullptr, nullptr, projhl, 512, 512, 2048, 512);
+    conv_mfma_r24<5><<<gT, 256, 0, stream>>>(xphl, wt5, c5b, cthl);
+    gemm_hl_r24<GF_ACCP><<<gT, 256, 0, stream>>>(cthl, mswhl + 1*512, nullptr, nullptr, nullptr, projhl, 512, 512, 2048, 512);
+    conv_mfma_r24<7><<<gT, 256, 0, stream>>>(xphl, wt7, c7b, cthl);
+    gemm_hl_r24<GF_ACCP><<<gT, 256, 0, stream>>>(cthl, mswhl + 2*512, nullptr, nullptr, nullptr, projhl, 512, 512, 2048, 512);
+    conv_mfma_r24<9><<<gT, 256, 0, stream>>>(xphl, wt9, c9b, cthl);
+    gemm_hl_r24<GF_ACCP><<<gT, 256, 0, stream>>>(cthl, mswhl + 3*512, nullptr, nullptr, nullptr, projhl, 512, 512, 2048, 512);
+
+    gemm_hl_r24<GF_BIAS><<<gT, 256, 0, stream>>>(projhl, inwkhl, inb + 512,  nullptr, nullptr, cthl, 512, 512, 512, 512);
+    gemm_hl_r24<GF_BIAS|GF_QSCALE><<<gT, 256, 0, stream>>>(projhl, inwqhl, inb, nullptr, nullptr, xphl, 512, 512, 512, 512);
+    gemm_hl_r24<GF_BIAS><<<gT, 256, 0, stream>>>(projhl, inwvhl, inb + 1024, nullptr, nullptr, vhl, 512, 512, 512, 512);
+
+    attn_mfma_r24<<<2048, 256, 0, stream>>>(xphl, cthl, vhl, xphl);
+
+    gemm_hl_r24<GF_BIAS|GF_ADDP><<<gT, 256, 0, stream>>>(xphl, aowhl, aob, nullptr, projhl, cthl, 512, 512, 512, 512);
+
+    row_sumsq_hl_r24<<<4096, 256, 0, stream>>>(cthl, asump);
+    row_sumsq_r24<<<512,  256, 0, stream>>>(cb, cbbp);
+    split_cb_r24<<<4096, 256, 0, stream>>>(cb, cbhl);
+    vq_argmin_mfma_r24<<<dim3(128, 4), 256, 0, stream>>>(cthl, cbhl, asump, cbbp, pbvp, pbip);
+    vq_reduce_r24<<<64, 256, 0, stream>>>(pbvp, pbip, idxp, out);
+    vq_loss_partial_r24<<<4096, 256, 0, stream>>>(cthl, cb, idxp, lpart);
+
+    gemm_bt_r24<GF_BIAS|GF_RELU><<<dim3(16, 2),  256, 0, stream>>>(cb, r1w, r1b, nullptr, nullptr, hregp, 512, 512, 512, 256);
+    gemm_bt_r24<GF_BIAS><<<dim3(16, 16), 256, 0, stream>>>(hregp, r2w, r2b, nullptr, nullptr, Rp, 256, 256, 256, 2048);
+    softmax_rows_r24<<<2048, 256, 0, stream>>>(Rp);
+    hash_table_r24<<<512, 256, 0, stream>>>(cb, hw, Tp);
+
+    write_loss_r24<<<1, 256, 0, stream>>>(lpart, out);
+    write_regime_r24<<<131072, 256, 0, stream>>>(Rp, idxp, out);
+    write_hash_r24<<<4096, 256, 0, stream>>>(Tp, idxp, out);
+    write_quant_r24<<<32768, 256, 0, stream>>>(cb, idxp, out);
+}
```

New measurement: 1.451 ms. Within noise of the previous version (-1.2%).
